# Kernel optimization log

Hardware: AMD Instinct MI355X
Metric: run time of the kernel (lower is better)

Reference implementation:

```python
import jax, jax.numpy as jnp
import numpy as np

DIM = 2048
HEAD_DIM = 64
NUM_HEADS = DIM // HEAD_DIM
ROT_DIM = HEAD_DIM // 2  # 32
THETA = 10000.0
LN_EPS = 1e-5


def setup_inputs() -> dict:
    key = jax.random.key(0)
    ks = jax.random.split(key, 6)
    n, s = 2, 2048
    x = jax.random.normal(ks[0], (n, s, DIM), dtype=jnp.float32)
    ln_w = jnp.ones((DIM,), dtype=jnp.float32)
    ln_b = jnp.zeros((DIM,), dtype=jnp.float32)
    # Linear weights stored as (in, out); torch Linear init scale ~ 1/sqrt(in)
    sc = 1.0 / np.sqrt(DIM)
    w_qkv = jax.random.uniform(ks[1], (DIM, 3 * DIM), jnp.float32, -sc, sc)
    b_qkv = jax.random.uniform(ks[2], (3 * DIM,), jnp.float32, -sc, sc)
    w_out = jax.random.uniform(ks[3], (DIM, DIM), jnp.float32, -sc, sc)
    b_out = jax.random.uniform(ks[4], (DIM,), jnp.float32, -sc, sc)
    return {"x": x, "ln_w": ln_w, "ln_b": ln_b, "w_qkv": w_qkv,
            "b_qkv": b_qkv, "w_out": w_out, "b_out": b_out}


def _rope_cos_sin(seq_len):
    # freqs: theta ** linspace(0, -1, rot_dim//2 + 1)[:-1] -> 16 freqs
    n_freq = ROT_DIM // 2
    exps = jnp.linspace(0.0, -1.0, n_freq + 1)[:-1]
    freqs = THETA ** exps  # [16]
    pos = jnp.arange(seq_len, dtype=jnp.float32)  # [s]
    tmp = pos[:, None] * freqs[None, :]  # [s, 16]
    # broadcast target: [1, 1, s, 16] over (n, h, s, d)
    return jnp.cos(tmp)[None, None], jnp.sin(tmp)[None, None]


def _apply_rotary(x, cos, sin):
    d = cos.shape[-1]  # 16
    x1, x2, x3 = x[..., :d], x[..., d:2 * d], x[..., 2 * d:]
    y1 = x1 * cos - x2 * sin
    y2 = x2 * cos + x1 * sin
    return jnp.concatenate([y1.astype(x3.dtype), y2.astype(x3.dtype), x3], axis=-1)


def reference(x, ln_w, ln_b, w_qkv, b_qkv, w_out, b_out):
    n, s, dim = x.shape
    skip = x
    # LayerNorm
    mu = jnp.mean(x, axis=-1, keepdims=True)
    var = jnp.var(x, axis=-1, keepdims=True)
    h = (x - mu) * jax.lax.rsqrt(var + LN_EPS) * ln_w + ln_b
    # fused QKV projection
    qkv = h @ w_qkv + b_qkv  # [n, s, 3*dim]
    qkv = qkv.reshape(n, s, 3, NUM_HEADS, HEAD_DIM)
    qkv = jnp.transpose(qkv, (2, 0, 3, 1, 4))  # [3, n, h, s, d]
    q, k, v = qkv[0], qkv[1], qkv[2]
    # RoPE on first rot_dim dims
    cos, sin = _rope_cos_sin(s)
    q = _apply_rotary(q, cos, sin)
    k = _apply_rotary(k, cos, sin)
    # causal SDPA
    scale = 1.0 / jnp.sqrt(jnp.asarray(HEAD_DIM, dtype=q.dtype))
    scores = jnp.einsum('nhqd,nhkd->nhqk', q, k) * scale
    causal = jnp.tril(jnp.ones((s, s), dtype=bool))
    scores = jnp.where(causal[None, None], scores, jnp.asarray(-jnp.inf, scores.dtype))
    attn = jax.nn.softmax(scores, axis=-1)
    o = jnp.einsum('nhqk,nhkd->nhqd', attn, v)  # [n, h, s, d]
    o = jnp.transpose(o, (0, 2, 1, 3)).reshape(n, s, dim)
    return o @ w_out + b_out + skip
```

## Files before the change

kernel.cpp:

```cpp
#include <hip/hip_runtime.h>
#include <hip/hip_bf16.h>
#include <cstdint>
#include <cstddef>

#define DIMM 2048
#define NHEADS 32
#define HDIM 64
#define SEQ 2048
#define NBATCH 2
#define ROWS 4096
#define NFREQ 16
#define NKT3 32

typedef __bf16 bfv8 __attribute__((ext_vector_type(8)));
typedef float f32x4v __attribute__((ext_vector_type(4)));
typedef float f32x16 __attribute__((ext_vector_type(16)));

__device__ __forceinline__ void gload16(const void* g, void* l) {
  __builtin_amdgcn_global_load_lds((const __attribute__((address_space(1))) void*)g,
                                   (__attribute__((address_space(3))) void*)l, 16, 0, 0);
}

__device__ __forceinline__ f32x4v mfma16(bfv8 a, bfv8 b, f32x4v c) {
  return __builtin_amdgcn_mfma_f32_16x16x32_bf16(a, b, c, 0, 0, 0);
}

__device__ __forceinline__ f32x16 mfma32(bfv8 a, bfv8 b, f32x16 c) {
  return __builtin_amdgcn_mfma_f32_32x32x16_bf16(a, b, c, 0, 0, 0);
}

__device__ __forceinline__ unsigned short f2bfu(float f) {
  __hip_bfloat16 h = __float2bfloat16(f);
  return __builtin_bit_cast(unsigned short, h);
}

__device__ __forceinline__ unsigned pack2bf(float a, float b) {
  return (unsigned)f2bfu(a) | ((unsigned)f2bfu(b) << 16);
}

__device__ __forceinline__ void swap32(unsigned& a, unsigned& b, const int hi) {
  const unsigned ta = (unsigned)__shfl_xor((int)a, 32);
  const unsigned tb = (unsigned)__shfl_xor((int)b, 32);
  const unsigned na = hi ? tb : a;
  const unsigned nb = hi ? b : ta;
  a = na;
  b = nb;
}

__device__ __forceinline__ void xcd_swizzle(int& bx, int& by) {
  const int gx = gridDim.x, nwg = gx * gridDim.y;
  const int orig = blockIdx.y * gx + blockIdx.x;
  const int q = nwg >> 3, r = nwg & 7;
  const int xcd = orig & 7, loc = orig >> 3;
  const int wg = (xcd < r ? xcd * (q + 1) : r * (q + 1) + (xcd - r) * q) + loc;
  bx = wg % gx;
  by = wg / gx;
}

__global__ __launch_bounds__(256) void rope_tab_kernel(float* __restrict__ ct,
                                                       float* __restrict__ st) {
  const int i = blockIdx.x * 256 + threadIdx.x;
  if (i >= SEQ * NFREQ) return;
  const int pos = i >> 4, f = i & 15;
  const float freq = powf(10000.0f, -(float)f / 16.0f);
  const float ang = (float)pos * freq;
  ct[i] = cosf(ang);
  st[i] = sinf(ang);
}

__global__ __launch_bounds__(256) void transpose_cast_kernel(const float* __restrict__ W,
                                                             __hip_bfloat16* __restrict__ WT,
                                                             int K, int N) {
  __shared__ float tile[32][33];
  const int n0 = blockIdx.x * 32, k0 = blockIdx.y * 32;
  const int tx = threadIdx.x, ty = threadIdx.y;
#pragma unroll
  for (int j = 0; j < 4; ++j)
    tile[ty + j * 8][tx] = W[(size_t)(k0 + ty + j * 8) * N + n0 + tx];
  __syncthreads();
#pragma unroll
  for (int j = 0; j < 4; ++j)
    WT[(size_t)(n0 + ty + j * 8) * K + k0 + tx] = __float2bfloat16(tile[tx][ty + j * 8]);
}

__global__ __launch_bounds__(256) void ln_kernel(const float* __restrict__ x,
                                                 const float* __restrict__ lw,
                                                 const float* __restrict__ lb,
                                                 __hip_bfloat16* __restrict__ h) {
  const int row = blockIdx.x;
  const int t = threadIdx.x;
  const float4* xr = (const float4*)(x + (size_t)row * DIMM);
  float4 a = xr[t * 2], b = xr[t * 2 + 1];
  float e[8];
  *(float4*)e = a; *(float4*)(e + 4) = b;
  float s = 0.f, ss = 0.f;
#pragma unroll
  for (int j = 0; j < 8; ++j) { s += e[j]; ss += e[j] * e[j]; }
#pragma unroll
  for (int o = 1; o < 64; o <<= 1) { s += __shfl_xor(s, o); ss += __shfl_xor(ss, o); }
  __shared__ float red[8];
  const int wid = t >> 6;
  if ((t & 63) == 0) { red[wid * 2] = s; red[wid * 2 + 1] = ss; }
  __syncthreads();
  s = red[0] + red[2] + red[4] + red[6];
  ss = red[1] + red[3] + red[5] + red[7];
  const float mu = s * (1.f / DIMM);
  const float var = ss * (1.f / DIMM) - mu * mu;
  const float rs = rsqrtf(var + 1e-5f);
  const float4* w4 = (const float4*)lw;
  const float4* b4 = (const float4*)lb;
  float4 wa = w4[t * 2], wb = w4[t * 2 + 1], ba = b4[t * 2], bb = b4[t * 2 + 1];
  float wv[8], bv[8];
  *(float4*)wv = wa; *(float4*)(wv + 4) = wb;
  *(float4*)bv = ba; *(float4*)(bv + 4) = bb;
  unsigned short hv[8];
#pragma unroll
  for (int j = 0; j < 8; ++j)
    hv[j] = f2bfu((e[j] - mu) * rs * wv[j] + bv[j]);
  *(uint4*)((char*)h + (size_t)row * (DIMM * 2) + t * 16) = *(uint4*)hv;
}

__device__ __forceinline__ void stageA64(const char* Ab, int brow, int kt,
                                         char* bufA, int c, int lane) {
  const int row = c * 8 + (lane >> 3);
  const int src = ((lane & 7) * 16) ^ ((row & 7) << 4);
  gload16(Ab + (size_t)(brow + row) * 4096 + kt * 128 + src, bufA + c * 1024);
}
__device__ __forceinline__ void stageB64(const char* Bb, int bcol, int kt,
                                         char* bufB, int c, int lane) {
  const int row = c * 8 + (lane >> 3);
  const int src = ((lane & 7) * 16) ^ ((row & 7) << 4);
  gload16(Bb + (size_t)(bcol + row) * 4096 + kt * 128 + src, bufB + c * 1024);
}

__device__ __forceinline__ void gemm_core3(const char* Ab, const char* Bb,
                                           int brow, int bcol, char* lds,
                                           f32x4v acc[8][4]) {
  const int tid = threadIdx.x, lane = tid & 63, wid = tid >> 6;
  const int g = lane >> 4, ln15 = lane & 15;
  const int wr = wid >> 2, wc = (wid >> 1) & 1, wk = wid & 1;
  const int kb = wk * 64;

#pragma unroll
  for (int t = 0; t < 2; ++t) {
    char* bufA = lds + t * 49152;
    char* bufB = bufA + 32768;
    stageA64(Ab, brow, t, bufA, wid, lane);
    stageA64(Ab, brow, t, bufA, wid + 8, lane);
    stageA64(Ab, brow, t, bufA, wid + 16, lane);
    stageA64(Ab, brow, t, bufA, wid + 24, lane);
    stageB64(Bb, bcol, t, bufB, wid, lane);
    stageB64(Bb, bcol, t, bufB, wid + 8, lane);
  }
  asm volatile("s_waitcnt vmcnt(6)" ::: "memory");
  __builtin_amdgcn_s_barrier();

  for (int t = 0; t < NKT3; ++t) {
    char* bufA = lds + (t % 3) * 49152;
    char* bufB = bufA + 32768;
    char* nbufA = lds + ((t + 2) % 3) * 49152;
    char* nbufB = nbufA + 32768;
    const bool st = (t + 2 < NKT3);
    bfv8 af[4], bfr[4];
#pragma unroll
    for (int mi = 0; mi < 4; ++mi) {
      const int ra = wr * 128 + mi * 16 + ln15;
      af[mi] = *(const bfv8*)(bufA + (size_t)ra * 128 + ((kb + g * 16) ^ ((ra & 7) << 4)));
    }
#pragma unroll
    for (int nf = 0; nf < 4; ++nf) {
      const int rb = wc * 64 + nf * 16 + ln15;
      bfr[nf] = *(const bfv8*)(bufB + (size_t)rb * 128 + ((kb + g * 16) ^ ((rb & 7) << 4)));
    }
    if (st) {
      stageA64(Ab, brow, t + 2, nbufA, wid, lane);
      stageA64(Ab, brow, t + 2, nbufA, wid + 8, lane);
      stageB64(Bb, bcol, t + 2, nbufB, wid, lane);
    }
    __builtin_amdgcn_s_setprio(1);
#pragma unroll
    for (int mi = 0; mi < 4; ++mi)
#pragma unroll
      for (int nf = 0; nf < 4; ++nf)
        acc[mi][nf] = mfma16(af[mi], bfr[nf], acc[mi][nf]);
    __builtin_amdgcn_s_setprio(0);
    bfv8 ao[4];
#pragma unroll
    for (int mi = 0; mi < 4; ++mi) {
      const int ra = wr * 128 + (4 + mi) * 16 + ln15;
      ao[mi] = *(const bfv8*)(bufA + (size_t)ra * 128 + ((kb + g * 16) ^ ((ra & 7) << 4)));
    }
    if (st) {
      stageA64(Ab, brow, t + 2, nbufA, wid + 16, lane);
      stageA64(Ab, brow, t + 2, nbufA, wid + 24, lane);
      stageB64(Bb, bcol, t + 2, nbufB, wid + 8, lane);
    }
    __builtin_amdgcn_s_setprio(1);
#pragma unroll
    for (int mi = 0; mi < 4; ++mi)
#pragma unroll
      for (int nf = 0; nf < 4; ++nf)
        acc[4 + mi][nf] = mfma16(ao[mi], bfr[nf], acc[4 + mi][nf]);
    __builtin_amdgcn_s_setprio(0);
    if (st) {
      asm volatile("s_waitcnt vmcnt(6)" ::: "memory");
    } else if (t == NKT3 - 2) {
      asm volatile("s_waitcnt vmcnt(0)" ::: "memory");
    }
    asm volatile("" ::: "memory");
    __builtin_amdgcn_s_barrier();
  }
}

__device__ __forceinline__ void kreduce(char* lds, f32x4v acc[8][4], f32x4v ak[4][4],
                                        int wid, int lane, int wk) {
  char* reg = lds + (size_t)wid * 16384;
#pragma unroll
  for (int q = 0; q < 4; ++q)
#pragma unroll
    for (int nf = 0; nf < 4; ++nf)
      *(f32x4v*)(reg + (q * 4 + nf) * 1024 + lane * 16) = acc[wk ? q : 4 + q][nf];
  __syncthreads();
  const char* preg = lds + (size_t)(wid ^ 1) * 16384;
#pragma unroll
  for (int q = 0; q < 4; ++q)
#pragma unroll
    for (int nf = 0; nf < 4; ++nf)
      ak[q][nf] = acc[wk ? 4 + q : q][nf] +
                  *(const f32x4v*)(preg + (q * 4 + nf) * 1024 + lane * 16);
  __syncthreads();
}

__global__ __launch_bounds__(512, 2) void gemm_qkv_kernel(
    const __hip_bfloat16* __restrict__ A, const __hip_bfloat16* __restrict__ BT,
    const float* __restrict__ bqkv, const float* __restrict__ ct, const float* __restrict__ st,
    __hip_bfloat16* __restrict__ qb, __hip_bfloat16* __restrict__ kb,
    __hip_bfloat16* __restrict__ vb) {
  __shared__ char lds[147456];
  const f32x4v fz = {0.f, 0.f, 0.f, 0.f};
  f32x4v acc[8][4];
#pragma unroll
  for (int mf = 0; mf < 8; ++mf)
#pragma unroll
    for (int nf = 0; nf < 4; ++nf) acc[mf][nf] = fz;
  int bx, by;
  xcd_swizzle(bx, by);
  const int brow = by * 256, bcol = bx * 128;
  gemm_core3((const char*)A, (const char*)BT, brow, bcol, lds, acc);

  const int tid = threadIdx.x, lane = tid & 63, wid = tid >> 6;
  const int g = lane >> 4, ln15 = lane & 15;
  const int wr = wid >> 2, wc = (wid >> 1) & 1, wk = wid & 1;
  f32x4v ak[4][4];
  kreduce(lds, acc, ak, wid, lane, wk);

  const int cb = bcol + wc * 64;
  const int which = cb >> 11;
  const int head = (cb & 2047) >> 6;
  const int rowbase = brow + wr * 128 + wk * 64;
  const int nidx = rowbase >> 11;
  const int posb = rowbase & 2047;
  float bias[4];
#pragma unroll
  for (int nf = 0; nf < 4; ++nf) bias[nf] = bqkv[cb + nf * 16 + ln15];

  if (which == 2) {
    char* tp = lds + wid * 8192;
    const size_t vhead = ((size_t)nidx * NHEADS + head) * (HDIM * SEQ);
#pragma unroll
    for (int q = 0; q < 4; ++q)
#pragma unroll
      for (int r = 0; r < 4; ++r) {
        const int posl = q * 16 + g * 4 + r;
#pragma unroll
        for (int nf = 0; nf < 4; ++nf) {
          const int d = nf * 16 + ln15;
          *(unsigned short*)(tp + d * 128 + ((posl * 2) ^ ((d & 7) << 4))) =
              f2bfu(ak[q][nf][r] + bias[nf]);
        }
      }
    asm volatile("s_waitcnt lgkmcnt(0)" ::: "memory");
    __builtin_amdgcn_sched_barrier(0);
#pragma unroll
    for (int i = 0; i < 8; ++i) {
      const int dl = i * 8 + (lane >> 3);
      const int cs = (lane & 7) ^ (dl & 7);
      const uint4 val = *(const uint4*)(tp + dl * 128 + cs * 16);
      *(uint4*)((char*)vb + (vhead + (size_t)dl * SEQ + posb + (lane & 7) * 8) * 2) = val;
    }
  } else {
    __hip_bfloat16* dst = (which == 0) ? qb : kb;
    char* tp = lds + wid * 8192;
#pragma unroll
    for (int q = 0; q < 4; ++q)
#pragma unroll
      for (int r = 0; r < 4; ++r) {
        const int posl = q * 16 + g * 4 + r;
        const int pos = posb + posl;
        float v0 = ak[q][0][r] + bias[0];
        float v1 = ak[q][1][r] + bias[1];
        float v2 = ak[q][2][r] + bias[2];
        float v3 = ak[q][3][r] + bias[3];
        const float c0 = ct[pos * 16 + ln15], s0 = st[pos * 16 + ln15];
        const float x1 = v0, x2 = v1;
        v0 = x1 * c0 - x2 * s0;
        v1 = x2 * c0 + x1 * s0;
        const int sw2 = (posl & 7) << 4;
        char* rowp = tp + posl * 128;
        *(unsigned short*)(rowp + ((ln15 * 2) ^ sw2)) = f2bfu(v0);
        *(unsigned short*)(rowp + ((32 + ln15 * 2) ^ sw2)) = f2bfu(v1);
        *(unsigned short*)(rowp + ((64 + ln15 * 2) ^ sw2)) = f2bfu(v2);
        *(unsigned short*)(rowp + ((96 + ln15 * 2) ^ sw2)) = f2bfu(v3);
      }
    asm volatile("s_waitcnt lgkmcnt(0)" ::: "memory");
    __builtin_amdgcn_sched_barrier(0);
    const size_t qkbase = (((size_t)(nidx * NHEADS + head)) * SEQ + posb) * HDIM;
#pragma unroll
    for (int i = 0; i < 8; ++i) {
      const int rr = i * 8 + (lane >> 3);
      const int cs = (lane & 7) ^ (rr & 7);
      const uint4 val = *(const uint4*)(tp + rr * 128 + cs * 16);
      *(uint4*)((char*)dst + (qkbase + (size_t)rr * HDIM) * 2 + (lane & 7) * 16) = val;
    }
  }
}

__global__ __launch_bounds__(512, 2) void gemm_out_kernel(
    const __hip_bfloat16* __restrict__ A, const __hip_bfloat16* __restrict__ BT,
    const float* __restrict__ bout, const float* __restrict__ skip,
    float* __restrict__ out) {
  __shared__ char lds[147456];
  const f32x4v fz = {0.f, 0.f, 0.f, 0.f};
  f32x4v acc[8][4];
#pragma unroll
  for (int mf = 0; mf < 8; ++mf)
#pragma unroll
    for (int nf = 0; nf < 4; ++nf) acc[mf][nf] = fz;
  int bx, by;
  xcd_swizzle(bx, by);
  const int brow = by * 256, bcol = bx * 128;
  gemm_core3((const char*)A, (const char*)BT, brow, bcol, lds, acc);

  const int tid = threadIdx.x, lane = tid & 63, wid = tid >> 6;
  const int g = lane >> 4, ln15 = lane & 15;
  const int wr = wid >> 2, wc = (wid >> 1) & 1, wk = wid & 1;
  f32x4v ak[4][4];
  kreduce(lds, acc, ak, wid, lane, wk);

  const int rowbase = brow + wr * 128 + wk * 64;
  char* tp = lds + wid * 16384;
#pragma unroll
  for (int q = 0; q < 4; ++q)
#pragma unroll
    for (int r = 0; r < 4; ++r) {
      const int posl = q * 16 + g * 4 + r;
      const int sw2 = ((posl >> 2) & 3) << 6;
      char* rowp = tp + posl * 256;
#pragma unroll
      for (int nf = 0; nf < 4; ++nf)
        *(float*)(rowp + ((nf * 64 + ln15 * 4) ^ sw2)) = ak[q][nf][r];
    }
  asm volatile("s_waitcnt lgkmcnt(0)" ::: "memory");
  __builtin_amdgcn_sched_barrier(0);
  const int colb = bcol + wc * 64;
#pragma unroll
  for (int i = 0; i < 16; ++i) {
    const int rr = i * 4 + (lane >> 4);
    const int cp = lane & 15;
    const float4 a4 = *(const float4*)(tp + rr * 256 + cp * 16);
    const int lc = (cp * 16) ^ (((rr >> 2) & 3) << 6);
    const int col = colb + (lc >> 2);
    const int row = rowbase + rr;
    const float4 sk = *(const float4*)(skip + (size_t)row * DIMM + col);
    const float4 bo = *(const float4*)(bout + col);
    float4 o4;
    o4.x = a4.x + sk.x + bo.x;
    o4.y = a4.y + sk.y + bo.y;
    o4.z = a4.z + sk.z + bo.z;
    o4.w = a4.w + sk.w + bo.w;
    *(float4*)(out + (size_t)row * DIMM + col) = o4;
  }
}

__global__ __launch_bounds__(256) void attn_kernel(
    const __hip_bfloat16* __restrict__ qb, const __hip_bfloat16* __restrict__ kb,
    const __hip_bfloat16* __restrict__ vtb, __hip_bfloat16* __restrict__ ob) {
  __shared__ char sm[33280];
  float* lred = (float*)(sm + 32768);
  const int tid = threadIdx.x, lane = tid & 63, wid = tid >> 6;
  const int ln31 = lane & 31, hi = lane >> 5;
  const int head = blockIdx.x;
  const int qbi = (int)gridDim.y - 1 - (int)blockIdx.y;
  const size_t hb = (size_t)head * (SEQ * HDIM);
  const int q0 = qbi * 128;
  const int qw = q0 + wid * 32;
  const int qg = qw + ln31;
  const int nt = qbi * 2 + 2;
  const char* Kg = (const char*)(kb + hb);
  const char* Vg = (const char*)(vtb + hb);

  bfv8 qf[4];
  {
    const char* Qp = (const char*)(qb + hb) + (size_t)(qw + ln31) * 128 + hi * 16;
#pragma unroll
    for (int j = 0; j < 4; ++j) qf[j] = *(const bfv8*)(Qp + j * 32);
  }

  f32x16 o0, o1;
#pragma unroll
  for (int i = 0; i < 16; ++i) { o0[i] = 0.f; o1[i] = 0.f; }
  float m_run = -1e30f, l_run = 0.f;
  const float scale = 0.125f;
  const int swz = (ln31 & 7) << 4;

#pragma unroll
  for (int i = 0; i < 2; ++i) {
    const int f = (tid + i * 256) * 16;
    const int row = f >> 7;
    const int src = (f & 127) ^ ((row & 7) << 4);
    gload16(Kg + (size_t)row * 128 + src, sm + f);
    gload16(Vg + (size_t)row * 4096 + src, sm + 16384 + f);
  }
  asm volatile("s_waitcnt vmcnt(0)" ::: "memory");
  __syncthreads();

  for (int t = 0; t < nt; ++t) {
    const int kvb = t * 64;
    if (t + 1 < nt) {
      const int nb = (t + 1) & 1;
      const int kvb2 = kvb + 64;
#pragma unroll
      for (int i = 0; i < 2; ++i) {
        const int f = (tid + i * 256) * 16;
        const int row = f >> 7;
        const int src = (f & 127) ^ ((row & 7) << 4);
        gload16(Kg + (size_t)(kvb2 + row) * 128 + src, sm + nb * 8192 + f);
        gload16(Vg + (size_t)row * 4096 + (size_t)kvb2 * 2 + src, sm + 16384 + nb * 8192 + f);
      }
    }
    if (kvb <= qw + 31) {
      const char* ldsK = sm + (t & 1) * 8192;
      const char* ldsV = sm + 16384 + (t & 1) * 8192;
      f32x16 s0, s1;
#pragma unroll
      for (int i = 0; i < 16; ++i) { s0[i] = 0.f; s1[i] = 0.f; }
      __builtin_amdgcn_s_setprio(1);
#pragma unroll
      for (int j = 0; j < 4; ++j) {
        const int byt = j * 32 + hi * 16;
        const bfv8 k0 = *(const bfv8*)(ldsK + ln31 * 128 + (byt ^ swz));
        const bfv8 k1 = *(const bfv8*)(ldsK + (32 + ln31) * 128 + (byt ^ swz));
        s0 = mfma32(k0, qf[j], s0);
        s1 = mfma32(k1, qf[j], s1);
      }
      __builtin_amdgcn_s_setprio(0);
      float p[32];
#pragma unroll
      for (int r = 0; r < 16; ++r) { p[r] = s0[r] * scale; p[16 + r] = s1[r] * scale; }
      if (kvb + 63 > qw) {
#pragma unroll
        for (int r = 0; r < 16; ++r) {
          const int kvo = (r & 3) + 8 * (r >> 2) + 4 * hi;
          if (kvb + kvo > qg) p[r] = -1e30f;
          if (kvb + 32 + kvo > qg) p[16 + r] = -1e30f;
        }
      }
      float mx = p[0];
#pragma unroll
      for (int r = 1; r < 32; ++r) mx = fmaxf(mx, p[r]);
      mx = fmaxf(mx, __shfl_xor(mx, 32));
      if (!__all(mx <= m_run + 8.0f)) {
        const float mn = fmaxf(m_run, mx);
        const float al = __expf(m_run - mn);
        m_run = mn;
        l_run *= al;
        lred[wid * 32 + ln31] = al;
        asm volatile("s_waitcnt lgkmcnt(0)" ::: "memory");
        __builtin_amdgcn_sched_barrier(0);
#pragma unroll
        for (int r = 0; r < 16; ++r) {
          const float a = lred[wid * 32 + (r & 3) + 8 * (r >> 2) + 4 * hi];
          o0[r] *= a;
          o1[r] *= a;
        }
      }
      float ps = 0.f;
#pragma unroll
      for (int r = 0; r < 32; ++r) { p[r] = __expf(p[r] - m_run); ps += p[r]; }
      ps += __shfl_xor(ps, 32);
      l_run += ps;
      unsigned c[16];
#pragma unroll
      for (int i = 0; i < 16; ++i) c[i] = pack2bf(p[2 * i], p[2 * i + 1]);
      bfv8 paf[4];
#pragma unroll
      for (int fI = 0; fI < 4; ++fI) {
        unsigned a0 = c[fI * 4 + 0], b0 = c[fI * 4 + 2];
        unsigned a1 = c[fI * 4 + 1], b1 = c[fI * 4 + 3];
        swap32(a0, b0, hi);
        swap32(a1, b1, hi);
        union { unsigned u[4]; bfv8 v; } w;
        w.u[0] = a0; w.u[1] = a1; w.u[2] = b0; w.u[3] = b1;
        paf[fI] = w.v;
      }
      __builtin_amdgcn_s_setprio(1);
#pragma unroll
      for (int ss = 0; ss < 4; ++ss) {
        const int byt = ss * 32 + hi * 16;
        const bfv8 v0 = *(const bfv8*)(ldsV + ln31 * 128 + (byt ^ swz));
        const bfv8 v1 = *(const bfv8*)(ldsV + (32 + ln31) * 128 + (byt ^ swz));
        o0 = mfma32(paf[ss], v0, o0);
        o1 = mfma32(paf[ss], v1, o1);
      }
      __builtin_amdgcn_s_setprio(0);
    }
    asm volatile("s_waitcnt vmcnt(0)" ::: "memory");
    __syncthreads();
  }

  lred[wid * 32 + ln31] = l_run;
  asm volatile("s_waitcnt lgkmcnt(0)" ::: "memory");
  __builtin_amdgcn_sched_barrier(0);
  const int nidx = head >> 5, hh = head & 31;
#pragma unroll
  for (int r = 0; r < 16; ++r) {
    const int qrow = qw + (r & 3) + 8 * (r >> 2) + 4 * hi;
    const float inv = 1.0f / lred[wid * 32 + (r & 3) + 8 * (r >> 2) + 4 * hi];
    __hip_bfloat16* dst = ob + ((size_t)nidx * SEQ + qrow) * DIMM + hh * 64;
    dst[ln31] = __float2bfloat16(o0[r] * inv);
    dst[32 + ln31] = __float2bfloat16(o1[r] * inv);
  }
}

extern "C" void kernel_launch(void* const* d_in, const int* in_sizes, int n_in,
                              void* d_out, int out_size, void* d_ws, size_t ws_size,
                              hipStream_t stream) {
  const float* x = (const float*)d_in[0];
  const float* ln_w = (const float*)d_in[1];
  const float* ln_b = (const float*)d_in[2];
  const float* w_qkv = (const float*)d_in[3];
  const float* b_qkv = (const float*)d_in[4];
  const float* w_out = (const float*)d_in[5];
  const float* b_out = (const float*)d_in[6];
  float* out = (float*)d_out;

  char* ws = (char*)d_ws;
  size_t off = 0;
  auto alloc = [&](size_t bytes) -> char* {
    char* p = ws + off;
    off += (bytes + 255) & ~(size_t)255;
    return p;
  };
  __hip_bfloat16* h = (__hip_bfloat16*)alloc((size_t)ROWS * DIMM * 2);
  __hip_bfloat16* wqkvT = (__hip_bfloat16*)alloc((size_t)3 * DIMM * DIMM * 2);
  __hip_bfloat16* woutT = (__hip_bfloat16*)alloc((size_t)DIMM * DIMM * 2);
  __hip_bfloat16* qbuf = (__hip_bfloat16*)alloc((size_t)ROWS * DIMM * 2);
  __hip_bfloat16* kbuf = (__hip_bfloat16*)alloc((size_t)ROWS * DIMM * 2);
  __hip_bfloat16* vtbuf = (__hip_bfloat16*)alloc((size_t)ROWS * DIMM * 2);
  __hip_bfloat16* obuf = (__hip_bfloat16*)alloc((size_t)ROWS * DIMM * 2);
  float* ct = (float*)alloc((size_t)SEQ * NFREQ * 4);
  float* st = (float*)alloc((size_t)SEQ * NFREQ * 4);

  rope_tab_kernel<<<dim3((SEQ * NFREQ + 255) / 256), dim3(256), 0, stream>>>(ct, st);
  transpose_cast_kernel<<<dim3(3 * DIMM / 32, DIMM / 32), dim3(32, 8), 0, stream>>>(
      w_qkv, wqkvT, DIMM, 3 * DIMM);
  transpose_cast_kernel<<<dim3(DIMM / 32, DIMM / 32), dim3(32, 8), 0, stream>>>(
      w_out, woutT, DIMM, DIMM);
  ln_kernel<<<dim3(ROWS), dim3(256), 0, stream>>>(x, ln_w, ln_b, h);
  gemm_qkv_kernel<<<dim3(3 * DIMM / 128, ROWS / 256), dim3(512), 0, stream>>>(
      h, wqkvT, b_qkv, ct, st, qbuf, kbuf, vtbuf);
  attn_kernel<<<dim3(NBATCH * NHEADS, SEQ / 128), dim3(256), 0, stream>>>(
      qbuf, kbuf, vtbuf, obuf);
  gemm_out_kernel<<<dim3(DIMM / 128, ROWS / 256), dim3(512), 0, stream>>>(
      obuf, woutT, b_out, x, out);
}
```

Before: 272.1 us.

## Rewrite QKV GEMM with 256x256 tiles, double-buffered LDS, no split-K

Replaces the QKV projection GEMM's 256x128 tile, which used intra-block split-K with an LDS reduction, with a 256x256 tile. Each of the 8 waves now owns a 128x64 output region over the full K. The new core double-buffers LDS and interleaves the next tile's global-to-LDS loads between four MFMA phases, raising priority during the MFMA bursts. The epilogue writes the two 64-row halves in turn through the same per-wave LDS scratch. This aims for more data reuse per load and removes the cross-wave reduction, at the cost of halving the grid (384 blocks) and adding extra barriers per k-step.

```diff
diff --git a/kernel.cpp b/kernel.cpp
--- a/kernel.cpp
+++ b/kernel.cpp
@@ -120,6 +120,245 @@
   *(uint4*)((char*)h + (size_t)row * (DIMM * 2) + t * 16) = *(uint4*)hv;
 }
 
+__device__ __forceinline__ void stage256(const char* base, int rowoff, int kt,
+                                         char* dst, int round, int tid) {
+  const int f = round * 8192 + tid * 16;
+  const int row = f >> 7;
+  const int src = (f & 127) ^ ((row & 7) << 4);
+  gload16(base + (size_t)(rowoff + row) * 4096 + kt * 128 + src, dst + f);
+}
+
+__device__ __forceinline__ void gemm256_core(const char* Ab, const char* Bb,
+                                             int brow, int bcol, char* lds,
+                                             f32x4v acc[8][4]) {
+  const int tid = threadIdx.x, lane = tid & 63, wid = tid >> 6;
+  const int g = lane >> 4, ln15 = lane & 15;
+  const int wr = wid >> 2, wc = wid & 3;
+
+#pragma unroll
+  for (int r2 = 0; r2 < 4; ++r2) stage256(Ab, brow, 0, lds, r2, tid);
+#pragma unroll
+  for (int r2 = 0; r2 < 4; ++r2) stage256(Bb, bcol, 0, lds + 32768, r2, tid);
+  asm volatile("s_waitcnt vmcnt(0)" ::: "memory");
+  __builtin_amdgcn_s_barrier();
+
+  for (int t = 0; t < NKT3; ++t) {
+    char* bufA = lds + (t & 1) * 65536;
+    char* bufB = bufA + 32768;
+    char* nA = lds + ((t + 1) & 1) * 65536;
+    char* nB = nA + 32768;
+    const bool st = (t + 1 < NKT3);
+    bfv8 a0[4][2], a4[4][2], b01[2][2], b23[2][2];
+#pragma unroll
+    for (int mi = 0; mi < 4; ++mi)
+#pragma unroll
+      for (int ks = 0; ks < 2; ++ks) {
+        const int ra = wr * 128 + mi * 16 + ln15;
+        a0[mi][ks] = *(const bfv8*)(bufA + (size_t)ra * 128 +
+                                    ((ks * 64 + g * 16) ^ ((ra & 7) << 4)));
+      }
+#pragma unroll
+    for (int nf = 0; nf < 2; ++nf)
+#pragma unroll
+      for (int ks = 0; ks < 2; ++ks) {
+        const int rb = wc * 64 + nf * 16 + ln15;
+        b01[nf][ks] = *(const bfv8*)(bufB + (size_t)rb * 128 +
+                                     ((ks * 64 + g * 16) ^ ((rb & 7) << 4)));
+      }
+    if (st) {
+      stage256(Ab, brow, t + 1, nA, 0, tid);
+      stage256(Ab, brow, t + 1, nA, 2, tid);
+      stage256(Bb, bcol, t + 1, nB, 0, tid);
+    }
+    __builtin_amdgcn_s_barrier();
+    asm volatile("s_waitcnt lgkmcnt(0)" ::: "memory");
+    __builtin_amdgcn_sched_barrier(0);
+    __builtin_amdgcn_s_setprio(1);
+#pragma unroll
+    for (int mi = 0; mi < 4; ++mi)
+#pragma unroll
+      for (int nf = 0; nf < 2; ++nf) {
+        acc[mi][nf] = mfma16(a0[mi][0], b01[nf][0], acc[mi][nf]);
+        acc[mi][nf] = mfma16(a0[mi][1], b01[nf][1], acc[mi][nf]);
+      }
+    __builtin_amdgcn_s_setprio(0);
+    __builtin_amdgcn_s_barrier();
+#pragma unroll
+    for (int nf = 0; nf < 2; ++nf)
+#pragma unroll
+      for (int ks = 0; ks < 2; ++ks) {
+        const int rb = wc * 64 + (2 + nf) * 16 + ln15;
+        b23[nf][ks] = *(const bfv8*)(bufB + (size_t)rb * 128 +
+                                     ((ks * 64 + g * 16) ^ ((rb & 7) << 4)));
+      }
+    if (st) {
+      stage256(Bb, bcol, t + 1, nB, 1, tid);
+      stage256(Bb, bcol, t + 1, nB, 2, tid);
+      stage256(Bb, bcol, t + 1, nB, 3, tid);
+    }
+    __builtin_amdgcn_s_barrier();
+    asm volatile("s_waitcnt lgkmcnt(0)" ::: "memory");
+    __builtin_amdgcn_sched_barrier(0);
+    __builtin_amdgcn_s_setprio(1);
+#pragma unroll
+    for (int mi = 0; mi < 4; ++mi)
+#pragma unroll
+      for (int nf = 0; nf < 2; ++nf) {
+        acc[mi][2 + nf] = mfma16(a0[mi][0], b23[nf][0], acc[mi][2 + nf]);
+        acc[mi][2 + nf] = mfma16(a0[mi][1], b23[nf][1], acc[mi][2 + nf]);
+      }
+    __builtin_amdgcn_s_setprio(0);
+    if (st) {
+      asm volatile("s_waitcnt vmcnt(6)" ::: "memory");
+    } else {
+      asm volatile("s_waitcnt vmcnt(0)" ::: "memory");
+    }
+    __builtin_amdgcn_s_barrier();
+#pragma unroll
+    for (int mi = 0; mi < 4; ++mi)
+#pragma unroll
+      for (int ks = 0; ks < 2; ++ks) {
+        const int ra = wr * 128 + (4 + mi) * 16 + ln15;
+        a4[mi][ks] = *(const bfv8*)(bufA + (size_t)ra * 128 +
+                                    ((ks * 64 + g * 16) ^ ((ra & 7) << 4)));
+      }
+    if (st) stage256(Ab, brow, t + 1, nA, 1, tid);
+    __builtin_amdgcn_s_barrier();
+    asm volatile("s_waitcnt lgkmcnt(0)" ::: "memory");
+    __builtin_amdgcn_sched_barrier(0);
+    __builtin_amdgcn_s_setprio(1);
+#pragma unroll
+    for (int mi = 0; mi < 4; ++mi)
+#pragma unroll
+      for (int nf = 0; nf < 2; ++nf) {
+        acc[4 + mi][nf] = mfma16(a4[mi][0], b01[nf][0], acc[4 + mi][nf]);
+        acc[4 + mi][nf] = mfma16(a4[mi][1], b01[nf][1], acc[4 + mi][nf]);
+      }
+    __builtin_amdgcn_s_setprio(0);
+    __builtin_amdgcn_s_barrier();
+    if (st) stage256(Ab, brow, t + 1, nA, 3, tid);
+    __builtin_amdgcn_s_setprio(1);
+#pragma unroll
+    for (int mi = 0; mi < 4; ++mi)
+#pragma unroll
+      for (int nf = 0; nf < 2; ++nf) {
+        acc[4 + mi][2 + nf] = mfma16(a4[mi][0], b23[nf][0], acc[4 + mi][2 + nf]);
+        acc[4 + mi][2 + nf] = mfma16(a4[mi][1], b23[nf][1], acc[4 + mi][2 + nf]);
+      }
+    __builtin_amdgcn_s_setprio(0);
+    if (st) {
+      asm volatile("s_waitcnt vmcnt(2)" ::: "memory");
+    }
+    __builtin_amdgcn_s_barrier();
+  }
+}
+
+__global__ __launch_bounds__(512, 2) void gemm_qkv_kernel(
+    const __hip_bfloat16* __restrict__ A, const __hip_bfloat16* __restrict__ BT,
+    const float* __restrict__ bqkv, const float* __restrict__ ct, const float* __restrict__ st,
+    __hip_bfloat16* __restrict__ qb, __hip_bfloat16* __restrict__ kb,
+    __hip_bfloat16* __restrict__ vb) {
+  __shared__ char lds[131072];
+  const f32x4v fz = {0.f, 0.f, 0.f, 0.f};
+  f32x4v acc[8][4];
+#pragma unroll
+  for (int mf = 0; mf < 8; ++mf)
+#pragma unroll
+    for (int nf = 0; nf < 4; ++nf) acc[mf][nf] = fz;
+  int bx, by;
+  xcd_swizzle(bx, by);
+  const int brow = by * 256, bcol = bx * 256;
+  gemm256_core((const char*)A, (const char*)BT, brow, bcol, lds, acc);
+
+  const int tid = threadIdx.x, lane = tid & 63, wid = tid >> 6;
+  const int g = lane >> 4, ln15 = lane & 15;
+  const int wr = wid >> 2, wc = wid & 3;
+  const int cb = bcol + wc * 64;
+  const int which = cb >> 11;
+  const int head = (cb & 2047) >> 6;
+  const int rowbase = brow + wr * 128;
+  const int nidx = rowbase >> 11;
+  float bias[4];
+#pragma unroll
+  for (int nf = 0; nf < 4; ++nf) bias[nf] = bqkv[cb + nf * 16 + ln15];
+
+  char* tp = lds + wid * 8192;
+  if (which == 2) {
+    const size_t vhead = ((size_t)nidx * NHEADS + head) * (HDIM * SEQ);
+#pragma unroll
+    for (int hm = 0; hm < 2; ++hm) {
+      if (hm == 1) {
+        asm volatile("s_waitcnt lgkmcnt(0)" ::: "memory");
+        __builtin_amdgcn_sched_barrier(0);
+      }
+#pragma unroll
+      for (int q = 0; q < 4; ++q)
+#pragma unroll
+        for (int r = 0; r < 4; ++r) {
+          const int posl = q * 16 + g * 4 + r;
+#pragma unroll
+          for (int nf = 0; nf < 4; ++nf) {
+            const int d = nf * 16 + ln15;
+            *(unsigned short*)(tp + d * 128 + ((posl * 2) ^ ((d & 7) << 4))) =
+                f2bfu(acc[hm * 4 + q][nf][r] + bias[nf]);
+          }
+        }
+      asm volatile("s_waitcnt lgkmcnt(0)" ::: "memory");
+      __builtin_amdgcn_sched_barrier(0);
+      const int posb = (rowbase & 2047) + hm * 64;
+#pragma unroll
+      for (int i = 0; i < 8; ++i) {
+        const int dl = i * 8 + (lane >> 3);
+        const int cs = (lane & 7) ^ (dl & 7);
+        const uint4 val = *(const uint4*)(tp + dl * 128 + cs * 16);
+        *(uint4*)((char*)vb + (vhead + (size_t)dl * SEQ + posb + (lane & 7) * 8) * 2) = val;
+      }
+    }
+  } else {
+    __hip_bfloat16* dst = (which == 0) ? qb : kb;
+    const size_t qkhead = ((size_t)(nidx * NHEADS + head)) * SEQ;
+#pragma unroll
+    for (int hm = 0; hm < 2; ++hm) {
+      if (hm == 1) {
+        asm volatile("s_waitcnt lgkmcnt(0)" ::: "memory");
+        __builtin_amdgcn_sched_barrier(0);
+      }
+      const int posb = (rowbase & 2047) + hm * 64;
+#pragma unroll
+      for (int q = 0; q < 4; ++q)
+#pragma unroll
+        for (int r = 0; r < 4; ++r) {
+          const int posl = q * 16 + g * 4 + r;
+          const int pos = posb + posl;
+          float v0 = acc[hm * 4 + q][0][r] + bias[0];
+          float v1 = acc[hm * 4 + q][1][r] + bias[1];
+          float v2 = acc[hm * 4 + q][2][r] + bias[2];
+          float v3 = acc[hm * 4 + q][3][r] + bias[3];
+          const float c0 = ct[pos * 16 + ln15], s0 = st[pos * 16 + ln15];
+          const float x1 = v0, x2 = v1;
+          v0 = x1 * c0 - x2 * s0;
+          v1 = x2 * c0 + x1 * s0;
+          const int sw2 = (posl & 7) << 4;
+          char* rowp = tp + posl * 128;
+          *(unsigned short*)(rowp + ((ln15 * 2) ^ sw2)) = f2bfu(v0);
+          *(unsigned short*)(rowp + ((32 + ln15 * 2) ^ sw2)) = f2bfu(v1);
+          *(unsigned short*)(rowp + ((64 + ln15 * 2) ^ sw2)) = f2bfu(v2);
+          *(unsigned short*)(rowp + ((96 + ln15 * 2) ^ sw2)) = f2bfu(v3);
+        }
+      asm volatile("s_waitcnt lgkmcnt(0)" ::: "memory");
+      __builtin_amdgcn_sched_barrier(0);
+      const size_t qkbase = (qkhead + posb) * HDIM;
+#pragma unroll
+      for (int i = 0; i < 8; ++i) {
+        const int rr = i * 8 + (lane >> 3);
+        const int cs = (lane & 7) ^ (rr & 7);
+        const uint4 val = *(const uint4*)(tp + rr * 128 + cs * 16);
+        *(uint4*)((char*)dst + (qkbase + (size_t)rr * HDIM) * 2 + (lane & 7) * 16) = val;
+      }
+    }
+  }
+}
+
 __device__ __forceinline__ void stageA64(const char* Ab, int brow, int kt,
                                          char* bufA, int c, int lane) {
   const int row = c * 8 + (lane >> 3);
@@ -140,7 +379,6 @@
   const int g = lane >> 4, ln15 = lane & 15;
   const int wr = wid >> 2, wc = (wid >> 1) & 1, wk = wid & 1;
   const int kb = wk * 64;
-
 #pragma unroll
   for (int t = 0; t < 2; ++t) {
     char* bufA = lds + t * 49152;
@@ -229,100 +467,6 @@
       ak[q][nf] = acc[wk ? 4 + q : q][nf] +
                   *(const f32x4v*)(preg + (q * 4 + nf) * 1024 + lane * 16);
   __syncthreads();
-}
-
-__global__ __launch_bounds__(512, 2) void gemm_qkv_kernel(
-    const __hip_bfloat16* __restrict__ A, const __hip_bfloat16* __restrict__ BT,
-    const float* __restrict__ bqkv, const float* __restrict__ ct, const float* __restrict__ st,
-    __hip_bfloat16* __restrict__ qb, __hip_bfloat16* __restrict__ kb,
-    __hip_bfloat16* __restrict__ vb) {
-  __shared__ char lds[147456];
-  const f32x4v fz = {0.f, 0.f, 0.f, 0.f};
-  f32x4v acc[8][4];
-#pragma unroll
-  for (int mf = 0; mf < 8; ++mf)
-#pragma unroll
-    for (int nf = 0; nf < 4; ++nf) acc[mf][nf] = fz;
-  int bx, by;
-  xcd_swizzle(bx, by);
-  const int brow = by * 256, bcol = bx * 128;
-  gemm_core3((const char*)A, (const char*)BT, brow, bcol, lds, acc);
-
-  const int tid = threadIdx.x, lane = tid & 63, wid = tid >> 6;
-  const int g = lane >> 4, ln15 = lane & 15;
-  const int wr = wid >> 2, wc = (wid >> 1) & 1, wk = wid & 1;
-  f32x4v ak[4][4];
-  kreduce(lds, acc, ak, wid, lane, wk);
-
-  const int cb = bcol + wc * 64;
-  const int which = cb >> 11;
-  const int head = (cb & 2047) >> 6;
-  const int rowbase = brow + wr * 128 + wk * 64;
-  const int nidx = rowbase >> 11;
-  const int posb = rowbase & 2047;
-  float bias[4];
-#pragma unroll
-  for (int nf = 0; nf < 4; ++nf) bias[nf] = bqkv[cb + nf * 16 + ln15];
-
-  if (which == 2) {
-    char* tp = lds + wid * 8192;
-    const size_t vhead = ((size_t)nidx * NHEADS + head) * (HDIM * SEQ);
-#pragma unroll
-    for (int q = 0; q < 4; ++q)
-#pragma unroll
-      for (int r = 0; r < 4; ++r) {
-        const int posl = q * 16 + g * 4 + r;
-#pragma unroll
-        for (int nf = 0; nf < 4; ++nf) {
-          const int d = nf * 16 + ln15;
-          *(unsigned short*)(tp + d * 128 + ((posl * 2) ^ ((d & 7) << 4))) =
-              f2bfu(ak[q][nf][r] + bias[nf]);
-        }
-      }
-    asm volatile("s_waitcnt lgkmcnt(0)" ::: "memory");
-    __builtin_amdgcn_sched_barrier(0);
-#pragma unroll
-    for (int i = 0; i < 8; ++i) {
-      const int dl = i * 8 + (lane >> 3);
-      const int cs = (lane & 7) ^ (dl & 7);
-      const uint4 val = *(const uint4*)(tp + dl * 128 + cs * 16);
-      *(uint4*)((char*)vb + (vhead + (size_t)dl * SEQ + posb + (lane & 7) * 8) * 2) = val;
-    }
-  } else {
-    __hip_bfloat16* dst = (which == 0) ? qb : kb;
-    char* tp = lds + wid * 8192;
-#pragma unroll
-    for (int q = 0; q < 4; ++q)
-#pragma unroll
-      for (int r = 0; r < 4; ++r) {
-        const int posl = q * 16 + g * 4 + r;
-        const int pos = posb + posl;
-        float v0 = ak[q][0][r] + bias[0];
-        float v1 = ak[q][1][r] + bias[1];
-        float v2 = ak[q][2][r] + bias[2];
-        float v3 = ak[q][3][r] + bias[3];
-        const float c0 = ct[pos * 16 + ln15], s0 = st[pos * 16 + ln15];
-        const float x1 = v0, x2 = v1;
-        v0 = x1 * c0 - x2 * s0;
-        v1 = x2 * c0 + x1 * s0;
-        const int sw2 = (posl & 7) << 4;
-        char* rowp = tp + posl * 128;
-        *(unsigned short*)(rowp + ((ln15 * 2) ^ sw2)) = f2bfu(v0);
-        *(unsigned short*)(rowp + ((32 + ln15 * 2) ^ sw2)) = f2bfu(v1);
-        *(unsigned short*)(rowp + ((64 + ln15 * 2) ^ sw2)) = f2bfu(v2);
-        *(unsigned short*)(rowp + ((96 + ln15 * 2) ^ sw2)) = f2bfu(v3);
-      }
-    asm volatile("s_waitcnt lgkmcnt(0)" ::: "memory");
-    __builtin_amdgcn_sched_barrier(0);
-    const size_t qkbase = (((size_t)(nidx * NHEADS + head)) * SEQ + posb) * HDIM;
-#pragma unroll
-    for (int i = 0; i < 8; ++i) {
-      const int rr = i * 8 + (lane >> 3);
-      const int cs = (lane & 7) ^ (rr & 7);
-      const uint4 val = *(const uint4*)(tp + rr * 128 + cs * 16);
-      *(uint4*)((char*)dst + (qkbase + (size_t)rr * HDIM) * 2 + (lane & 7) * 16) = val;
-    }
-  }
 }
 
 __global__ __launch_bounds__(512, 2) void gemm_out_kernel(
@@ -567,7 +711,7 @@
   transpose_cast_kernel<<<dim3(DIMM / 32, DIMM / 32), dim3(32, 8), 0, stream>>>(
       w_out, woutT, DIMM, DIMM);
   ln_kernel<<<dim3(ROWS), dim3(256), 0, stream>>>(x, ln_w, ln_b, h);
-  gemm_qkv_kernel<<<dim3(3 * DIMM / 128, ROWS / 256), dim3(512), 0, stream>>>(
+  gemm_qkv_kernel<<<dim3(3 * DIMM / 256, ROWS / 256), dim3(512), 0, stream>>>(
       h, wqkvT, b_qkv, ct, st, qbuf, kbuf, vtbuf);
   attn_kernel<<<dim3(NBATCH * NHEADS, SEQ / 128), dim3(256), 0, stream>>>(
       qbuf, kbuf, vtbuf, obuf);
```

New measurement: 274.7 us. Within noise of the previous version (+1.0%).
